# Performance work log

Hardware: AMD Instinct MI355X
Metric: run time of the kernel (lower is better)

The kernel has to match this reference:

```python
import jax, jax.numpy as jnp
import numpy as np

N = 50000
E = 800000
F_IN = 128
HID = 64
NEG_SLOPE = 0.2
LN_EPS = 1e-5


def _gat_layer(x, W, att_src, att_dst, bias, src, dst, heads, out_ch, concat):
    # x: [N, in], W: [in, heads*out_ch], att_*: [heads, out_ch]
    n = x.shape[0]
    xp = (x @ W).reshape(n, heads, out_ch)                    # [N, H, C]
    a_src = jnp.einsum('nhc,hc->nh', xp, att_src)             # [N, H]
    a_dst = jnp.einsum('nhc,hc->nh', xp, att_dst)             # [N, H]
    e = jax.nn.leaky_relu(a_src[src] + a_dst[dst], NEG_SLOPE) # [E, H]
    # edge softmax over incoming edges of each destination node
    m = jax.ops.segment_max(e, dst, num_segments=n)           # [N, H]
    ex = jnp.exp(e - m[dst])
    s = jax.ops.segment_sum(ex, dst, num_segments=n)          # [N, H]
    alpha = ex / s[dst]                                       # [E, H]
    agg = jax.ops.segment_sum(xp[src] * alpha[:, :, None], dst, num_segments=n)
    out = agg.reshape(n, heads * out_ch) if concat else agg.mean(axis=1)
    return out + bias


def _layernorm(x, g, b):
    mu = x.mean(-1, keepdims=True)
    var = x.var(-1, keepdims=True)
    return (x - mu) / jnp.sqrt(var + LN_EPS) * g + b


def setup_inputs() -> dict:
    key = jax.random.key(0)
    ks = jax.random.split(key, 12)
    sc = 0.1
    return {
        'x': jax.random.normal(ks[0], (N, F_IN), jnp.float32),
        'edge_index': jax.random.randint(ks[1], (2, E), 0, N, jnp.int64),
        'W1': jax.random.normal(ks[2], (F_IN, 4 * HID), jnp.float32) * sc,
        'att_src1': jax.random.normal(ks[3], (4, HID), jnp.float32) * sc,
        'att_dst1': jax.random.normal(ks[4], (4, HID), jnp.float32) * sc,
        'b1': jnp.zeros((4 * HID,), jnp.float32),
        'ln1_g': jnp.ones((4 * HID,), jnp.float32),
        'ln1_b': jnp.zeros((4 * HID,), jnp.float32),
        'W2': jax.random.normal(ks[5], (4 * HID, 2 * HID), jnp.float32) * sc,
        'att_src2': jax.random.normal(ks[6], (2, HID), jnp.float32) * sc,
        'att_dst2': jax.random.normal(ks[7], (2, HID), jnp.float32) * sc,
        'b2': jnp.zeros((2 * HID,), jnp.float32),
        'ln2_g': jnp.ones((2 * HID,), jnp.float32),
        'ln2_b': jnp.zeros((2 * HID,), jnp.float32),
        'W3': jax.random.normal(ks[8], (2 * HID, F_IN), jnp.float32) * sc,
        'att_src3': jax.random.normal(ks[9], (1, F_IN), jnp.float32) * sc,
        'att_dst3': jax.random.normal(ks[10], (1, F_IN), jnp.float32) * sc,
        'b3': jnp.zeros((F_IN,), jnp.float32),
    }


def reference(x, edge_index, W1, att_src1, att_dst1, b1, ln1_g, ln1_b,
              W2, att_src2, att_dst2, b2, ln2_g, ln2_b,
              W3, att_src3, att_dst3, b3):
    n = x.shape[0]
    # PyG GATConv default: add self-loops
    loop = jnp.arange(n, dtype=edge_index.dtype)
    src = jnp.concatenate([edge_index[0], loop])
    dst = jnp.concatenate([edge_index[1], loop])

    h = _gat_layer(x, W1, att_src1, att_dst1, b1, src, dst, 4, HID, True)
    h = jax.nn.elu(_layernorm(h, ln1_g, ln1_b))
    # dropout p=0.2 is identity in eval mode
    h = _gat_layer(h, W2, att_src2, att_dst2, b2, src, dst, 2, HID, True)
    h = jax.nn.elu(_layernorm(h, ln2_g, ln2_b))
    out = _gat_layer(h, W3, att_src3, att_dst3, b3, src, dst, 1, F_IN, True)
    return out
```

## Files before the change

### kernel.cpp

```cpp
#include <hip/hip_runtime.h>
#include <hip/hip_bf16.h>
#include <math.h>

#define N_NODES 50000
#define N_EDGES 800000
#define E_TOT   850000
#define SCAN_B  1024

typedef __hip_bfloat16 bf16;
typedef __attribute__((ext_vector_type(8))) short short8v;
typedef __attribute__((ext_vector_type(4))) float float4v;

static __device__ __forceinline__ float u2f(unsigned short u) {
    return __uint_as_float(((unsigned int)u) << 16);
}
static __device__ __forceinline__ unsigned short f2u(float f) {
    unsigned int u = __float_as_uint(f);
    return (unsigned short)((u + 0x7FFFu + ((u >> 16) & 1u)) >> 16);
}

template<bool BF>
static __device__ __forceinline__ float ldv(const void* p, int i) {
    if constexpr (BF)
        return u2f(((const unsigned short*)p)[i]);
    else
        return ((const float*)p)[i];
}

__global__ void k_detect(const unsigned int* __restrict__ x32,
                         const unsigned int* __restrict__ ei32,
                         int* __restrict__ flags) {
    if (threadIdx.x == 0 && blockIdx.x == 0) {
        int cnt = 0;
        for (int i = 0; i < 256; i++) {
            unsigned int e = (x32[i] >> 7) & 0xFF;
            cnt += (e >= 90 && e <= 140) ? 1 : 0;
        }
        flags[0] = (cnt >= 128) ? 1 : 0;
        int z = 0;
        for (int i = 0; i < 64; i++) z += (ei32[2 * i + 1] == 0) ? 1 : 0;
        flags[1] = (z >= 48) ? 1 : 0;
    }
}

__global__ void k_zero(int* __restrict__ p, int n) {
    int i = blockIdx.x * blockDim.x + threadIdx.x;
    if (i < n) p[i] = 0;
}

template<bool I64>
__global__ void k_hist(const int* __restrict__ flags, const void* __restrict__ ei,
                       int* __restrict__ counts) {
    if ((flags[1] != 0) != I64) return;
    int i = blockIdx.x * blockDim.x + threadIdx.x;
    if (i >= E_TOT) return;
    int d;
    if (i < N_EDGES)
        d = I64 ? (int)((const long long*)ei)[N_EDGES + i] : ((const int*)ei)[N_EDGES + i];
    else
        d = i - N_EDGES;
    atomicAdd(&counts[d], 1);
}

__global__ void k_scan1(const int* __restrict__ counts, int* __restrict__ scanned,
                        int* __restrict__ partial, int n) {
    __shared__ int sh[SCAN_B];
    int i = blockIdx.x * SCAN_B + threadIdx.x;
    sh[threadIdx.x] = (i < n) ? counts[i] : 0;
    __syncthreads();
    for (int off = 1; off < SCAN_B; off <<= 1) {
        int t = (threadIdx.x >= off) ? sh[threadIdx.x - off] : 0;
        __syncthreads();
        sh[threadIdx.x] += t;
        __syncthreads();
    }
    if (i < n) scanned[i] = sh[threadIdx.x];
    if (threadIdx.x == SCAN_B - 1) partial[blockIdx.x] = sh[SCAN_B - 1];
}

__global__ void k_scan2(int* __restrict__ partial, int nb) {
    if (threadIdx.x == 0 && blockIdx.x == 0) {
        int acc = 0;
        for (int b = 0; b < nb; b++) { int t = partial[b]; partial[b] = acc; acc += t; }
    }
}

__global__ void k_scan3(const int* __restrict__ counts, const int* __restrict__ scanned,
                        const int* __restrict__ partial, int* __restrict__ rowptr,
                        int* __restrict__ cursor, int n) {
    int i = blockIdx.x * blockDim.x + threadIdx.x;
    if (i >= n) return;
    int incl = scanned[i] + partial[i / SCAN_B];
    rowptr[i + 1] = incl;
    cursor[i]     = incl - counts[i];
    if (i == 0) rowptr[0] = 0;
}

template<bool I64>
__global__ void k_scatter(const int* __restrict__ flags, const void* __restrict__ ei,
                          int* __restrict__ cursor, int* __restrict__ csr_src) {
    if ((flags[1] != 0) != I64) return;
    int i = blockIdx.x * blockDim.x + threadIdx.x;
    if (i >= E_TOT) return;
    int s, d;
    if (i < N_EDGES) {
        if constexpr (I64) {
            s = (int)((const long long*)ei)[i];
            d = (int)((const long long*)ei)[N_EDGES + i];
        } else {
            s = ((const int*)ei)[i];
            d = ((const int*)ei)[N_EDGES + i];
        }
    } else {
        s = d = i - N_EDGES;
    }
    int pos = atomicAdd(&cursor[d], 1);
    csr_src[pos] = s;
}

template<bool XBF>
__global__ void k_prepx(const int* __restrict__ flags, const void* __restrict__ x,
                        bf16* __restrict__ xb, int n4) {
    if ((flags[0] != 0) != XBF) return;
    int i = blockIdx.x * blockDim.x + threadIdx.x;
    if (i >= n4) return;
    if constexpr (XBF) {
        ((ushort4*)xb)[i] = ((const ushort4*)x)[i];
    } else {
        float4 f = ((const float4*)x)[i];
        ushort4 u;
        u.x = f2u(f.x); u.y = f2u(f.y); u.z = f2u(f.z); u.w = f2u(f.w);
        ((ushort4*)xb)[i] = u;
    }
}

template<int K, int NT, bool PBF>
__global__ void k_prepw(const int* __restrict__ flags, const void* __restrict__ W,
                        bf16* __restrict__ Wt) {
    if ((flags[0] != 0) != PBF) return;
    int i = blockIdx.x * blockDim.x + threadIdx.x;
    if (i >= K * NT) return;
    int k = i / NT, c = i - k * NT;
    Wt[c * K + k] = __float2bfloat16(ldv<PBF>(W, i));
}

struct PrepArgs { const void* src[13]; int off[13]; int len[13]; };

template<bool PBF>
__global__ void k_prep_small(const int* __restrict__ flags, PrepArgs a,
                             float* __restrict__ par) {
    if ((flags[0] != 0) != PBF) return;
    for (int seg = blockIdx.x; seg < 13; seg += gridDim.x)
        for (int i = threadIdx.x; i < a.len[seg]; i += blockDim.x)
            par[a.off[seg] + i] = ldv<PBF>(a.src[seg], i);
}

template<int K, int NT, int SPW, int H>
__global__ __launch_bounds__(256) void k_gemm_mfma2(const bf16* __restrict__ A,
                                                    const bf16* __restrict__ Wt,
                                                    bf16* __restrict__ xp,
                                                    const float* __restrict__ att_s,
                                                    const float* __restrict__ att_d,
                                                    float* __restrict__ asr,
                                                    float* __restrict__ adst) {
    constexpr int KF     = K / 32;
    constexpr int NSG    = NT / (16 * SPW);
    constexpr int NTILES = N_NODES / 16;
    constexpr int C      = NT / H;
    const int l    = threadIdx.x & 63;
    const int wid  = blockIdx.x * 4 + (threadIdx.x >> 6);
    const int sg   = wid % NSG;
    const int wpg  = (gridDim.x * 4) / NSG;
    const int t0   = wid / NSG;
    const int r16  = l & 15;
    const int kgrp = (l >> 4) * 8;
    const int head = (sg * SPW * 16) / C;

    short8v b[SPW][KF];
    float as_r[SPW][4], ad_r[SPW][4];
    #pragma unroll
    for (int s = 0; s < SPW; s++) {
        const int cs  = (sg * SPW + s) * 16;
        const int col = cs + r16;
        #pragma unroll
        for (int kf = 0; kf < KF; kf++)
            b[s][kf] = *(const short8v*)(Wt + (size_t)col * K + kf * 32 + kgrp);
        #pragma unroll
        for (int r = 0; r < 4; r++) {
            const int ch = cs + (l >> 4) * 4 + r;
            as_r[s][r] = att_s[ch];
            ad_r[s][r] = att_d[ch];
        }
    }

    for (int t = t0; t < NTILES; t += wpg) {
        const int m0 = t * 16;
        short8v a[KF];
        #pragma unroll
        for (int kf = 0; kf < KF; kf++)
            a[kf] = *(const short8v*)(A + (size_t)(m0 + r16) * K + kf * 32 + kgrp);
        float4v acc[SPW] = {};
        #pragma unroll
        for (int kf = 0; kf < KF; kf++)
            #pragma unroll
            for (int s = 0; s < SPW; s++)
                acc[s] = __builtin_amdgcn_mfma_f32_16x16x32_bf16(b[s][kf], a[kf], acc[s], 0, 0, 0);

        float pa = 0.f, pd = 0.f;
        #pragma unroll
        for (int s = 0; s < SPW; s++)
            #pragma unroll
            for (int r = 0; r < 4; r++) {
                pa = fmaf(acc[s][r], as_r[s][r], pa);
                pd = fmaf(acc[s][r], ad_r[s][r], pd);
            }
        pa += __shfl_xor(pa, 16); pa += __shfl_xor(pa, 32);
        pd += __shfl_xor(pd, 16); pd += __shfl_xor(pd, 32);
        if (l < 16) {
            atomicAdd(&asr [(size_t)(m0 + l) * H + head], pa);
            atomicAdd(&adst[(size_t)(m0 + l) * H + head], pd);
        }

        const int node = m0 + r16;
        #pragma unroll
        for (int s = 0; s < SPW; s++) {
            const int ch = (sg * SPW + s) * 16 + (l >> 4) * 4;
            uint2 o;
            o.x = (unsigned int)f2u(acc[s][0]) | ((unsigned int)f2u(acc[s][1]) << 16);
            o.y = (unsigned int)f2u(acc[s][2]) | ((unsigned int)f2u(acc[s][3]) << 16);
            *(uint2*)(xp + (size_t)node * NT + ch) = o;
        }
    }
}

template<int ND>
static __device__ __forceinline__ void gacc(const unsigned int* __restrict__ xpd,
                                            int off, float a, float* __restrict__ acc) {
    unsigned int d[ND];
    if constexpr (ND == 4) {
        uint4 t = *(const uint4*)(xpd + off);
        d[0] = t.x; d[1] = t.y; d[2] = t.z; d[3] = t.w;
    } else {
        uint2 t = *(const uint2*)(xpd + off);
        d[0] = t.x; d[1] = t.y;
    }
    #pragma unroll
    for (int k = 0; k < ND; k++) {
        acc[2 * k]     = fmaf(a, __uint_as_float(d[k] << 16),         acc[2 * k]);
        acc[2 * k + 1] = fmaf(a, __uint_as_float(d[k] & 0xffff0000u), acc[2 * k + 1]);
    }
}

template<int CT, int H, bool LAST, bool OBF>
__global__ __launch_bounds__(256) void k_agg3(const int* __restrict__ flags,
                                              const bf16* __restrict__ xp,
                                              const float* __restrict__ asr,
                                              const float* __restrict__ adst,
                                              const int* __restrict__ rowptr,
                                              const int* __restrict__ csr_src,
                                              const float* __restrict__ bias,
                                              const float* __restrict__ gamma,
                                              const float* __restrict__ beta,
                                              void* __restrict__ outv) {
    if constexpr (LAST) { if ((flags[0] != 0) != OBF) return; }
    constexpr int NPW = 2;
    constexpr int LPN = 64 / NPW;
    constexpr int V   = CT / LPN;
    constexpr int C   = CT / H;
    constexpr int LPH = C / V;
    constexpr int ND  = V / 2;
    constexpr int STR = CT / 2;
    const int l     = threadIdx.x & 63;
    const int w     = threadIdx.x >> 6;
    const int half  = l / LPN;
    const int li    = l - half * LPN;
    const int hd    = li / LPH;
    const int slot  = li & (LPH - 1);
    const int lbase = half * LPN + hd * LPH;
    const int coff  = ND * li;

    float bv[V], gv[V], bev[V];
    #pragma unroll
    for (int v = 0; v < V; v++) bv[v] = bias[V * li + v];
    if constexpr (!LAST) {
        #pragma unroll
        for (int v = 0; v < V; v++) {
            gv[v]  = gamma[V * li + v];
            bev[v] = beta [V * li + v];
        }
    }
    const unsigned int* xpd = (const unsigned int*)xp;

    for (int n0 = blockIdx.x * 4 + w; n0 * NPW < N_NODES; n0 += gridDim.x * 4) {
        const int n  = n0 * NPW + half;
        const int b0 = rowptr[n], b1 = rowptr[n + 1];
        const int deg = b1 - b0;
        const float ad = adst[n * H + hd];

        float m = -1e30f, s = 0.f;
        for (int j = b0 + slot; j < b1; j += LPH) {
            int sn = csr_src[j];
            float e = asr[sn * H + hd] + ad;
            e = e > 0.f ? e : 0.2f * e;
            float mn = fmaxf(m, e);
            s = s * __expf(m - mn) + __expf(e - mn);
            m = mn;
        }
        #pragma unroll
        for (int off = 1; off < LPH; off <<= 1) {
            float mo = __shfl_xor(m, off);
            float so = __shfl_xor(s, off);
            float mn = fmaxf(m, mo);
            s = s * __expf(m - mn) + so * __expf(mo - mn);
            m = mn;
        }
        const float inv_s = 1.f / s;

        float acc[V];
        #pragma unroll
        for (int v = 0; v < V; v++) acc[v] = 0.f;

        for (int cbase = 0; cbase < deg; cbase += LPH) {
            const int nn = min(LPH, deg - cbase);
            int   sn_l = 0;
            float al_l = 0.f;
            if (slot < nn) {
                sn_l = csr_src[b0 + cbase + slot];
                float e = asr[sn_l * H + hd] + ad;
                e = e > 0.f ? e : 0.2f * e;
                al_l = __expf(e - m) * inv_s;
            }
            const int nn4 = (nn + 3) & ~3;
            for (int e4 = 0; e4 < nn4; e4 += 4) {
                int   s0 = __shfl(sn_l, lbase + e4 + 0);
                int   s1 = __shfl(sn_l, lbase + e4 + 1);
                int   s2 = __shfl(sn_l, lbase + e4 + 2);
                int   s3 = __shfl(sn_l, lbase + e4 + 3);
                float a0 = __shfl(al_l, lbase + e4 + 0);
                float a1 = __shfl(al_l, lbase + e4 + 1);
                float a2 = __shfl(al_l, lbase + e4 + 2);
                float a3 = __shfl(al_l, lbase + e4 + 3);
                gacc<ND>(xpd, s0 * STR + coff, a0, acc);
                gacc<ND>(xpd, s1 * STR + coff, a1, acc);
                gacc<ND>(xpd, s2 * STR + coff, a2, acc);
                gacc<ND>(xpd, s3 * STR + coff, a3, acc);
            }
        }
        #pragma unroll
        for (int v = 0; v < V; v++) acc[v] += bv[v];

        if constexpr (!LAST) {
            float lsum = 0.f, lsq = 0.f;
            #pragma unroll
            for (int v = 0; v < V; v++) { lsum += acc[v]; lsq = fmaf(acc[v], acc[v], lsq); }
            #pragma unroll
            for (int off = 1; off < LPN; off <<= 1) {
                lsum += __shfl_xor(lsum, off);
                lsq  += __shfl_xor(lsq,  off);
            }
            float mu  = lsum * (1.f / CT);
            float var = lsq  * (1.f / CT) - mu * mu;
            float rs  = rsqrtf(var + 1e-5f);
            unsigned int od[ND];
            #pragma unroll
            for (int k = 0; k < ND; k++) {
                float y0 = (acc[2 * k]     - mu) * rs * gv[2 * k]     + bev[2 * k];
                float y1 = (acc[2 * k + 1] - mu) * rs * gv[2 * k + 1] + bev[2 * k + 1];
                y0 = y0 > 0.f ? y0 : expm1f(y0);
                y1 = y1 > 0.f ? y1 : expm1f(y1);
                od[k] = (unsigned int)f2u(y0) | ((unsigned int)f2u(y1) << 16);
            }
            unsigned int* ob = (unsigned int*)outv + (size_t)n * STR + coff;
            if constexpr (ND == 4) *(uint4*)ob = make_uint4(od[0], od[1], od[2], od[3]);
            else                   *(uint2*)ob = make_uint2(od[0], od[1]);
        } else {
            if constexpr (OBF) {
                uint2 o;
                o.x = (unsigned int)f2u(acc[0]) | ((unsigned int)f2u(acc[1]) << 16);
                o.y = (unsigned int)f2u(acc[2]) | ((unsigned int)f2u(acc[3]) << 16);
                *(uint2*)((bf16*)outv + (size_t)n * CT + V * li) = o;
            } else {
                *(float4*)((float*)outv + (size_t)n * CT + V * li) =
                    make_float4(acc[0], acc[1], acc[2], acc[3]);
            }
        }
    }
}

extern "C" void kernel_launch(void* const* d_in, const int* in_sizes, int n_in,
                              void* d_out, int out_size, void* d_ws, size_t ws_size,
                              hipStream_t stream) {
    const void* x   = d_in[0];
    const void* ei  = d_in[1];
    const void* W1  = d_in[2];
    const void* W2  = d_in[8];
    const void* W3  = d_in[14];

    char* ws = (char*)d_ws;
    bf16*  xp     = (bf16*)(ws);
    bf16*  hbuf   = (bf16*)(ws + 25600000);
    float* asr    = (float*)(ws + 51200000);
    float* adst   = (float*)(ws + 52000000);
    int*   counts = (int*)  (ws + 52800000);
    int*   scannd = (int*)  (ws + 53000000);
    int*   part   = (int*)  (ws + 53200000);
    int*   rowptr = (int*)  (ws + 53200256);
    int*   cursor = (int*)  (ws + 53400260);
    int*   csrsrc = (int*)  (ws + 53600260);
    int*   flags  = (int*)  (ws + 57000260);
    bf16*  Wt1    = (bf16*)(ws + 57000320);
    bf16*  Wt2    = (bf16*)(ws + 57065856);
    bf16*  Wt3    = (bf16*)(ws + 57131392);
    float* params = (float*)(ws + 57164160);

    bf16* xb = hbuf;

    const int nb_scan = (N_NODES + SCAN_B - 1) / SCAN_B;
    const int AGGB    = (N_NODES / 2 + 3) / 4;

    k_detect<<<1, 64, 0, stream>>>((const unsigned int*)x, (const unsigned int*)ei, flags);

    k_zero<<<(N_NODES + 255) / 256, 256, 0, stream>>>(counts, N_NODES);
    k_hist<false><<<(E_TOT + 255) / 256, 256, 0, stream>>>(flags, ei, counts);
    k_hist<true ><<<(E_TOT + 255) / 256, 256, 0, stream>>>(flags, ei, counts);
    k_scan1<<<nb_scan, SCAN_B, 0, stream>>>(counts, scannd, part, N_NODES);
    k_scan2<<<1, 64, 0, stream>>>(part, nb_scan);
    k_scan3<<<(N_NODES + 255) / 256, 256, 0, stream>>>(counts, scannd, part, rowptr, cursor, N_NODES);
    k_scatter<false><<<(E_TOT + 255) / 256, 256, 0, stream>>>(flags, ei, cursor, csrsrc);
    k_scatter<true ><<<(E_TOT + 255) / 256, 256, 0, stream>>>(flags, ei, cursor, csrsrc);

    const int n4 = N_NODES * 128 / 4;
    k_prepx<false><<<(n4 + 255) / 256, 256, 0, stream>>>(flags, x, xb, n4);
    k_prepx<true ><<<(n4 + 255) / 256, 256, 0, stream>>>(flags, x, xb, n4);
    k_prepw<128, 256, false><<<128, 256, 0, stream>>>(flags, W1, Wt1);
    k_prepw<128, 256, true ><<<128, 256, 0, stream>>>(flags, W1, Wt1);
    k_prepw<256, 128, false><<<128, 256, 0, stream>>>(flags, W2, Wt2);
    k_prepw<256, 128, true ><<<128, 256, 0, stream>>>(flags, W2, Wt2);
    k_prepw<128, 128, false><<<64, 256, 0, stream>>>(flags, W3, Wt3);
    k_prepw<128, 128, true ><<<64, 256, 0, stream>>>(flags, W3, Wt3);

    PrepArgs pa;
    const int srcs[13] = {3, 4, 5, 6, 7, 9, 10, 11, 12, 13, 15, 16, 17};
    const int offs[13] = {0, 256, 512, 768, 1024, 1280, 1408, 1536, 1664, 1792, 1920, 2048, 2176};
    const int lens[13] = {256, 256, 256, 256, 256, 128, 128, 128, 128, 128, 128, 128, 128};
    for (int i = 0; i < 13; i++) { pa.src[i] = d_in[srcs[i]]; pa.off[i] = offs[i]; pa.len[i] = lens[i]; }
    k_prep_small<false><<<13, 256, 0, stream>>>(flags, pa, params);
    k_prep_small<true ><<<13, 256, 0, stream>>>(flags, pa, params);

    k_zero<<<(400000 + 255) / 256, 256, 0, stream>>>((int*)asr, 400000);
    k_gemm_mfma2<128, 256, 4, 4><<<768, 256, 0, stream>>>(xb, Wt1, xp, params + 0, params + 256, asr, adst);
    k_agg3<256, 4, false, false><<<AGGB, 256, 0, stream>>>(flags, xp, asr, adst, rowptr, csrsrc,
                                                           params + 512, params + 768, params + 1024, hbuf);

    k_zero<<<(400000 + 255) / 256, 256, 0, stream>>>((int*)asr, 400000);
    k_gemm_mfma2<256, 128, 2, 2><<<768, 256, 0, stream>>>(hbuf, Wt2, xp, params + 1280, params + 1408, asr, adst);
    k_agg3<128, 2, false, false><<<AGGB, 256, 0, stream>>>(flags, xp, asr, adst, rowptr, csrsrc,
                                                           params + 1536, params + 1664, params + 1792, hbuf);

    k_zero<<<(400000 + 255) / 256, 256, 0, stream>>>((int*)asr, 400000);
    k_gemm_mfma2<128, 128, 2, 1><<<768, 256, 0, stream>>>(hbuf, Wt3, xp, params + 1920, params + 2048, asr, adst);
    k_agg3<128, 1, true, false><<<AGGB, 256, 0, stream>>>(flags, xp, asr, adst, rowptr, csrsrc,
                                                          params + 2176, nullptr, nullptr, d_out);
    k_agg3<128, 1, true, true ><<<AGGB, 256, 0, stream>>>(flags, xp, asr, adst, rowptr, csrsrc,
                                                          params + 2176, nullptr, nullptr, d_out);
}
```

Baseline: 354.8 us.

## Degree-sort aggregation nodes, store fp16 projections, merge prep kernels and zeroing

Nodes are bucketed by in-degree and processed in descending-degree order, so the two nodes sharing a wavefront have similar work and load imbalance drops. Projected features are stored as fp16 instead of bf16, and the aggregation loop now batches 4-8 gathers before accumulating to expose more memory-level parallelism. Duplicate flag-dispatched kernel launches are collapsed into runtime branches, the per-layer zero kernels are merged into one init kernel with separate attention buffers per layer, and weight preparation runs as one kernel. The extra degree-sort kernels add setup cost, and fp16 storage changes overflow and rounding behaviour.

```diff
diff --git a/kernel.cpp b/kernel.cpp
--- a/kernel.cpp
+++ b/kernel.cpp
@@ -1,11 +1,13 @@
 #include <hip/hip_runtime.h>
 #include <hip/hip_bf16.h>
+#include <hip/hip_fp16.h>
 #include <math.h>
 
 #define N_NODES 50000
 #define N_EDGES 800000
 #define E_TOT   850000
 #define SCAN_B  1024
+#define NPAIRS  (N_NODES / 2)
 
 typedef __hip_bfloat16 bf16;
 typedef __attribute__((ext_vector_type(8))) short short8v;
@@ -18,45 +20,39 @@
     unsigned int u = __float_as_uint(f);
     return (unsigned short)((u + 0x7FFFu + ((u >> 16) & 1u)) >> 16);
 }
-
-template<bool BF>
-static __device__ __forceinline__ float ldv(const void* p, int i) {
-    if constexpr (BF)
-        return u2f(((const unsigned short*)p)[i]);
-    else
-        return ((const float*)p)[i];
-}
-
-__global__ void k_detect(const unsigned int* __restrict__ x32,
-                         const unsigned int* __restrict__ ei32,
-                         int* __restrict__ flags) {
-    if (threadIdx.x == 0 && blockIdx.x == 0) {
-        int cnt = 0;
-        for (int i = 0; i < 256; i++) {
-            unsigned int e = (x32[i] >> 7) & 0xFF;
-            cnt += (e >= 90 && e <= 140) ? 1 : 0;
-        }
-        flags[0] = (cnt >= 128) ? 1 : 0;
-        int z = 0;
-        for (int i = 0; i < 64; i++) z += (ei32[2 * i + 1] == 0) ? 1 : 0;
-        flags[1] = (z >= 48) ? 1 : 0;
-    }
-}
-
-__global__ void k_zero(int* __restrict__ p, int n) {
-    int i = blockIdx.x * blockDim.x + threadIdx.x;
-    if (i < n) p[i] = 0;
-}
-
-template<bool I64>
+static __device__ __forceinline__ float ldr(const void* p, int i, bool bf) {
+    return bf ? u2f(((const unsigned short*)p)[i]) : ((const float*)p)[i];
+}
+
+__global__ void k_init(const unsigned int* __restrict__ x32,
+                       const unsigned int* __restrict__ ei32,
+                       int* __restrict__ zero_base, int nzero,
+                       int* __restrict__ flags) {
+    int i = blockIdx.x * 256 + threadIdx.x;
+    if (i < nzero) zero_base[i] = 0;
+    if (blockIdx.x == 0) {
+        __shared__ int c1, c2;
+        if (threadIdx.x == 0) { c1 = 0; c2 = 0; }
+        __syncthreads();
+        unsigned int e = (x32[threadIdx.x] >> 7) & 0xFF;
+        if (e >= 90 && e <= 140) atomicAdd(&c1, 1);
+        if (threadIdx.x < 64 && ei32[2 * threadIdx.x + 1] == 0) atomicAdd(&c2, 1);
+        __syncthreads();
+        if (threadIdx.x == 0) {
+            flags[0] = (c1 >= 128) ? 1 : 0;
+            flags[1] = (c2 >= 48) ? 1 : 0;
+        }
+    }
+}
+
 __global__ void k_hist(const int* __restrict__ flags, const void* __restrict__ ei,
                        int* __restrict__ counts) {
-    if ((flags[1] != 0) != I64) return;
     int i = blockIdx.x * blockDim.x + threadIdx.x;
     if (i >= E_TOT) return;
     int d;
     if (i < N_EDGES)
-        d = I64 ? (int)((const long long*)ei)[N_EDGES + i] : ((const int*)ei)[N_EDGES + i];
+        d = flags[1] ? (int)((const long long*)ei)[N_EDGES + i]
+                     : ((const int*)ei)[N_EDGES + i];
     else
         d = i - N_EDGES;
     atomicAdd(&counts[d], 1);
@@ -87,24 +83,39 @@
 
 __global__ void k_scan3(const int* __restrict__ counts, const int* __restrict__ scanned,
                         const int* __restrict__ partial, int* __restrict__ rowptr,
-                        int* __restrict__ cursor, int n) {
+                        int* __restrict__ cursor, int* __restrict__ dhist, int n) {
     int i = blockIdx.x * blockDim.x + threadIdx.x;
     if (i >= n) return;
     int incl = scanned[i] + partial[i / SCAN_B];
     rowptr[i + 1] = incl;
     cursor[i]     = incl - counts[i];
     if (i == 0) rowptr[0] = 0;
-}
-
-template<bool I64>
+    atomicAdd(&dhist[min(counts[i], 511)], 1);
+}
+
+__global__ void k_dscan(const int* __restrict__ dhist, int* __restrict__ dbase) {
+    if (threadIdx.x == 0 && blockIdx.x == 0) {
+        int acc = 0;
+        for (int d = 511; d >= 0; d--) { dbase[d] = acc; acc += dhist[d]; }
+    }
+}
+
+__global__ void k_dscatter(const int* __restrict__ counts, const int* __restrict__ dbase,
+                           int* __restrict__ dcur, int* __restrict__ order) {
+    int i = blockIdx.x * blockDim.x + threadIdx.x;
+    if (i >= N_NODES) return;
+    int deg = min(counts[i], 511);
+    int pos = dbase[deg] + atomicAdd(&dcur[deg], 1);
+    order[pos] = i;
+}
+
 __global__ void k_scatter(const int* __restrict__ flags, const void* __restrict__ ei,
                           int* __restrict__ cursor, int* __restrict__ csr_src) {
-    if ((flags[1] != 0) != I64) return;
     int i = blockIdx.x * blockDim.x + threadIdx.x;
     if (i >= E_TOT) return;
     int s, d;
     if (i < N_EDGES) {
-        if constexpr (I64) {
+        if (flags[1]) {
             s = (int)((const long long*)ei)[i];
             d = (int)((const long long*)ei)[N_EDGES + i];
         } else {
@@ -118,13 +129,11 @@
     csr_src[pos] = s;
 }
 
-template<bool XBF>
 __global__ void k_prepx(const int* __restrict__ flags, const void* __restrict__ x,
                         bf16* __restrict__ xb, int n4) {
-    if ((flags[0] != 0) != XBF) return;
     int i = blockIdx.x * blockDim.x + threadIdx.x;
     if (i >= n4) return;
-    if constexpr (XBF) {
+    if (flags[0]) {
         ((ushort4*)xb)[i] = ((const ushort4*)x)[i];
     } else {
         float4 f = ((const float4*)x)[i];
@@ -134,31 +143,39 @@
     }
 }
 
-template<int K, int NT, bool PBF>
-__global__ void k_prepw(const int* __restrict__ flags, const void* __restrict__ W,
-                        bf16* __restrict__ Wt) {
-    if ((flags[0] != 0) != PBF) return;
-    int i = blockIdx.x * blockDim.x + threadIdx.x;
-    if (i >= K * NT) return;
-    int k = i / NT, c = i - k * NT;
-    Wt[c * K + k] = __float2bfloat16(ldv<PBF>(W, i));
+__global__ void k_prepw_all(const int* __restrict__ flags,
+                            const void* __restrict__ W1, const void* __restrict__ W2,
+                            const void* __restrict__ W3,
+                            bf16* __restrict__ Wt1, bf16* __restrict__ Wt2,
+                            bf16* __restrict__ Wt3) {
+    const bool bf = flags[0] != 0;
+    int i = blockIdx.x * 256 + threadIdx.x;
+    if (i < 32768) {
+        int k = i >> 8, c = i & 255;
+        Wt1[c * 128 + k] = __float2bfloat16(ldr(W1, i, bf));
+    } else if (i < 65536) {
+        int j = i - 32768, k = j >> 7, c = j & 127;
+        Wt2[c * 256 + k] = __float2bfloat16(ldr(W2, j, bf));
+    } else if (i < 81920) {
+        int j = i - 65536, k = j >> 7, c = j & 127;
+        Wt3[c * 128 + k] = __float2bfloat16(ldr(W3, j, bf));
+    }
 }
 
 struct PrepArgs { const void* src[13]; int off[13]; int len[13]; };
 
-template<bool PBF>
 __global__ void k_prep_small(const int* __restrict__ flags, PrepArgs a,
                              float* __restrict__ par) {
-    if ((flags[0] != 0) != PBF) return;
+    const bool bf = flags[0] != 0;
     for (int seg = blockIdx.x; seg < 13; seg += gridDim.x)
         for (int i = threadIdx.x; i < a.len[seg]; i += blockDim.x)
-            par[a.off[seg] + i] = ldv<PBF>(a.src[seg], i);
+            par[a.off[seg] + i] = ldr(a.src[seg], i, bf);
 }
 
 template<int K, int NT, int SPW, int H>
 __global__ __launch_bounds__(256) void k_gemm_mfma2(const bf16* __restrict__ A,
                                                     const bf16* __restrict__ Wt,
-                                                    bf16* __restrict__ xp,
+                                                    unsigned short* __restrict__ xp,
                                                     const float* __restrict__ att_s,
                                                     const float* __restrict__ att_d,
                                                     float* __restrict__ asr,
@@ -226,57 +243,41 @@
         for (int s = 0; s < SPW; s++) {
             const int ch = (sg * SPW + s) * 16 + (l >> 4) * 4;
             uint2 o;
-            o.x = (unsigned int)f2u(acc[s][0]) | ((unsigned int)f2u(acc[s][1]) << 16);
-            o.y = (unsigned int)f2u(acc[s][2]) | ((unsigned int)f2u(acc[s][3]) << 16);
+            o.x = (unsigned int)__half_as_ushort(__float2half(acc[s][0])) |
+                  ((unsigned int)__half_as_ushort(__float2half(acc[s][1])) << 16);
+            o.y = (unsigned int)__half_as_ushort(__float2half(acc[s][2])) |
+                  ((unsigned int)__half_as_ushort(__float2half(acc[s][3])) << 16);
             *(uint2*)(xp + (size_t)node * NT + ch) = o;
         }
     }
 }
 
-template<int ND>
-static __device__ __forceinline__ void gacc(const unsigned int* __restrict__ xpd,
-                                            int off, float a, float* __restrict__ acc) {
-    unsigned int d[ND];
-    if constexpr (ND == 4) {
-        uint4 t = *(const uint4*)(xpd + off);
-        d[0] = t.x; d[1] = t.y; d[2] = t.z; d[3] = t.w;
-    } else {
-        uint2 t = *(const uint2*)(xpd + off);
-        d[0] = t.x; d[1] = t.y;
-    }
-    #pragma unroll
-    for (int k = 0; k < ND; k++) {
-        acc[2 * k]     = fmaf(a, __uint_as_float(d[k] << 16),         acc[2 * k]);
-        acc[2 * k + 1] = fmaf(a, __uint_as_float(d[k] & 0xffff0000u), acc[2 * k + 1]);
-    }
-}
-
-template<int CT, int H, bool LAST, bool OBF>
-__global__ __launch_bounds__(256) void k_agg3(const int* __restrict__ flags,
-                                              const bf16* __restrict__ xp,
+template<int CT, int H, bool LAST>
+__global__ __launch_bounds__(256) void k_agg4(const int* __restrict__ flags,
+                                              const unsigned short* __restrict__ xp,
                                               const float* __restrict__ asr,
                                               const float* __restrict__ adst,
                                               const int* __restrict__ rowptr,
                                               const int* __restrict__ csr_src,
+                                              const int* __restrict__ order,
                                               const float* __restrict__ bias,
                                               const float* __restrict__ gamma,
                                               const float* __restrict__ beta,
                                               void* __restrict__ outv) {
-    if constexpr (LAST) { if ((flags[0] != 0) != OBF) return; }
-    constexpr int NPW = 2;
-    constexpr int LPN = 64 / NPW;
+    constexpr int LPN = 32;
     constexpr int V   = CT / LPN;
     constexpr int C   = CT / H;
     constexpr int LPH = C / V;
     constexpr int ND  = V / 2;
     constexpr int STR = CT / 2;
+    constexpr int G   = (ND == 4) ? 4 : 8;
     const int l     = threadIdx.x & 63;
     const int w     = threadIdx.x >> 6;
-    const int half  = l / LPN;
-    const int li    = l - half * LPN;
+    const int half  = l >> 5;
+    const int li    = l & 31;
     const int hd    = li / LPH;
     const int slot  = li & (LPH - 1);
-    const int lbase = half * LPN + hd * LPH;
+    const int lbase = half * 32 + hd * LPH;
     const int coff  = ND * li;
 
     float bv[V], gv[V], bev[V];
@@ -291,14 +292,25 @@
     }
     const unsigned int* xpd = (const unsigned int*)xp;
 
-    for (int n0 = blockIdx.x * 4 + w; n0 * NPW < N_NODES; n0 += gridDim.x * 4) {
-        const int n  = n0 * NPW + half;
-        const int b0 = rowptr[n], b1 = rowptr[n + 1];
-        const int deg = b1 - b0;
-        const float ad = adst[n * H + hd];
-
-        float m = -1e30f, s = 0.f;
-        for (int j = b0 + slot; j < b1; j += LPH) {
+    const int p = blockIdx.x * 4 + w;
+    if (p >= NPAIRS) return;
+    const int n  = order[2 * p + half];
+    const int b0 = rowptr[n], b1 = rowptr[n + 1];
+    const int deg = b1 - b0;
+    const float ad = adst[n * H + hd];
+    const int sn_first = csr_src[b0];
+
+    float m, s, e0 = 0.f;
+    int sn0 = sn_first;
+    {
+        int j = b0 + slot;
+        if (j < b1) {
+            sn0 = csr_src[j];
+            float e = asr[sn0 * H + hd] + ad;
+            e0 = e > 0.f ? e : 0.2f * e;
+            m = e0; s = 1.f;
+        } else { m = -1e30f; s = 0.f; }
+        for (j += LPH; j < b1; j += LPH) {
             int sn = csr_src[j];
             float e = asr[sn * H + hd] + ad;
             e = e > 0.f ? e : 0.2f * e;
@@ -306,83 +318,99 @@
             s = s * __expf(m - mn) + __expf(e - mn);
             m = mn;
         }
-        #pragma unroll
-        for (int off = 1; off < LPH; off <<= 1) {
-            float mo = __shfl_xor(m, off);
-            float so = __shfl_xor(s, off);
-            float mn = fmaxf(m, mo);
-            s = s * __expf(m - mn) + so * __expf(mo - mn);
-            m = mn;
-        }
-        const float inv_s = 1.f / s;
-
-        float acc[V];
-        #pragma unroll
-        for (int v = 0; v < V; v++) acc[v] = 0.f;
-
-        for (int cbase = 0; cbase < deg; cbase += LPH) {
-            const int nn = min(LPH, deg - cbase);
-            int   sn_l = 0;
-            float al_l = 0.f;
-            if (slot < nn) {
+    }
+    #pragma unroll
+    for (int off = 1; off < LPH; off <<= 1) {
+        float mo = __shfl_xor(m, off);
+        float so = __shfl_xor(s, off);
+        float mn = fmaxf(m, mo);
+        s = s * __expf(m - mn) + so * __expf(mo - mn);
+        m = mn;
+    }
+    const float inv_s = 1.f / s;
+
+    float acc[V];
+    #pragma unroll
+    for (int v = 0; v < V; v++) acc[v] = 0.f;
+
+    for (int cbase = 0; cbase < deg; cbase += LPH) {
+        const int nn = min(LPH, deg - cbase);
+        int   sn_l = sn_first;
+        float al_l = 0.f;
+        if (slot < nn) {
+            if (cbase == 0) {
+                sn_l = sn0;
+                al_l = __expf(e0 - m) * inv_s;
+            } else {
                 sn_l = csr_src[b0 + cbase + slot];
                 float e = asr[sn_l * H + hd] + ad;
                 e = e > 0.f ? e : 0.2f * e;
                 al_l = __expf(e - m) * inv_s;
             }
-            const int nn4 = (nn + 3) & ~3;
-            for (int e4 = 0; e4 < nn4; e4 += 4) {
-                int   s0 = __shfl(sn_l, lbase + e4 + 0);
-                int   s1 = __shfl(sn_l, lbase + e4 + 1);
-                int   s2 = __shfl(sn_l, lbase + e4 + 2);
-                int   s3 = __shfl(sn_l, lbase + e4 + 3);
-                float a0 = __shfl(al_l, lbase + e4 + 0);
-                float a1 = __shfl(al_l, lbase + e4 + 1);
-                float a2 = __shfl(al_l, lbase + e4 + 2);
-                float a3 = __shfl(al_l, lbase + e4 + 3);
-                gacc<ND>(xpd, s0 * STR + coff, a0, acc);
-                gacc<ND>(xpd, s1 * STR + coff, a1, acc);
-                gacc<ND>(xpd, s2 * STR + coff, a2, acc);
-                gacc<ND>(xpd, s3 * STR + coff, a3, acc);
+        }
+        const int nnG = (nn + G - 1) & ~(G - 1);
+        for (int eb = 0; eb < nnG; eb += G) {
+            int sns[G]; float als[G];
+            #pragma unroll
+            for (int g = 0; g < G; g++) {
+                sns[g] = __shfl(sn_l, lbase + eb + g);
+                als[g] = __shfl(al_l, lbase + eb + g);
             }
-        }
-        #pragma unroll
-        for (int v = 0; v < V; v++) acc[v] += bv[v];
-
-        if constexpr (!LAST) {
-            float lsum = 0.f, lsq = 0.f;
+            unsigned int d[G][ND];
             #pragma unroll
-            for (int v = 0; v < V; v++) { lsum += acc[v]; lsq = fmaf(acc[v], acc[v], lsq); }
+            for (int g = 0; g < G; g++) {
+                if constexpr (ND == 4)
+                    *(uint4*)d[g] = *(const uint4*)(xpd + (size_t)sns[g] * STR + coff);
+                else
+                    *(uint2*)d[g] = *(const uint2*)(xpd + (size_t)sns[g] * STR + coff);
+            }
             #pragma unroll
-            for (int off = 1; off < LPN; off <<= 1) {
-                lsum += __shfl_xor(lsum, off);
-                lsq  += __shfl_xor(lsq,  off);
-            }
-            float mu  = lsum * (1.f / CT);
-            float var = lsq  * (1.f / CT) - mu * mu;
-            float rs  = rsqrtf(var + 1e-5f);
-            unsigned int od[ND];
-            #pragma unroll
-            for (int k = 0; k < ND; k++) {
-                float y0 = (acc[2 * k]     - mu) * rs * gv[2 * k]     + bev[2 * k];
-                float y1 = (acc[2 * k + 1] - mu) * rs * gv[2 * k + 1] + bev[2 * k + 1];
-                y0 = y0 > 0.f ? y0 : expm1f(y0);
-                y1 = y1 > 0.f ? y1 : expm1f(y1);
-                od[k] = (unsigned int)f2u(y0) | ((unsigned int)f2u(y1) << 16);
-            }
-            unsigned int* ob = (unsigned int*)outv + (size_t)n * STR + coff;
-            if constexpr (ND == 4) *(uint4*)ob = make_uint4(od[0], od[1], od[2], od[3]);
-            else                   *(uint2*)ob = make_uint2(od[0], od[1]);
+            for (int g = 0; g < G; g++)
+                #pragma unroll
+                for (int k = 0; k < ND; k++) {
+                    float x0 = __half2float(__ushort_as_half((unsigned short)(d[g][k] & 0xffffu)));
+                    float x1 = __half2float(__ushort_as_half((unsigned short)(d[g][k] >> 16)));
+                    acc[2 * k]     = fmaf(als[g], x0, acc[2 * k]);
+                    acc[2 * k + 1] = fmaf(als[g], x1, acc[2 * k + 1]);
+                }
+        }
+    }
+    #pragma unroll
+    for (int v = 0; v < V; v++) acc[v] += bv[v];
+
+    if constexpr (!LAST) {
+        float lsum = 0.f, lsq = 0.f;
+        #pragma unroll
+        for (int v = 0; v < V; v++) { lsum += acc[v]; lsq = fmaf(acc[v], acc[v], lsq); }
+        #pragma unroll
+        for (int off = 1; off < LPN; off <<= 1) {
+            lsum += __shfl_xor(lsum, off);
+            lsq  += __shfl_xor(lsq,  off);
+        }
+        float mu  = lsum * (1.f / CT);
+        float var = lsq  * (1.f / CT) - mu * mu;
+        float rs  = rsqrtf(var + 1e-5f);
+        unsigned int od[ND];
+        #pragma unroll
+        for (int k = 0; k < ND; k++) {
+            float y0 = (acc[2 * k]     - mu) * rs * gv[2 * k]     + bev[2 * k];
+            float y1 = (acc[2 * k + 1] - mu) * rs * gv[2 * k + 1] + bev[2 * k + 1];
+            y0 = y0 > 0.f ? y0 : expm1f(y0);
+            y1 = y1 > 0.f ? y1 : expm1f(y1);
+            od[k] = (unsigned int)f2u(y0) | ((unsigned int)f2u(y1) << 16);
+        }
+        unsigned int* ob = (unsigned int*)outv + (size_t)n * STR + coff;
+        if constexpr (ND == 4) *(uint4*)ob = make_uint4(od[0], od[1], od[2], od[3]);
+        else                   *(uint2*)ob = make_uint2(od[0], od[1]);
+    } else {
+        if (flags[0]) {
+            uint2 o;
+            o.x = (unsigned int)f2u(acc[0]) | ((unsigned int)f2u(acc[1]) << 16);
+            o.y = (unsigned int)f2u(acc[2]) | ((unsigned int)f2u(acc[3]) << 16);
+            *(uint2*)((bf16*)outv + (size_t)n * CT + V * li) = o;
         } else {
-            if constexpr (OBF) {
-                uint2 o;
-                o.x = (unsigned int)f2u(acc[0]) | ((unsigned int)f2u(acc[1]) << 16);
-                o.y = (unsigned int)f2u(acc[2]) | ((unsigned int)f2u(acc[3]) << 16);
-                *(uint2*)((bf16*)outv + (size_t)n * CT + V * li) = o;
-            } else {
-                *(float4*)((float*)outv + (size_t)n * CT + V * li) =
-                    make_float4(acc[0], acc[1], acc[2], acc[3]);
-            }
+            *(float4*)((float*)outv + (size_t)n * CT + V * li) =
+                make_float4(acc[0], acc[1], acc[2], acc[3]);
         }
     }
 }
@@ -390,77 +418,72 @@
 extern "C" void kernel_launch(void* const* d_in, const int* in_sizes, int n_in,
                               void* d_out, int out_size, void* d_ws, size_t ws_size,
                               hipStream_t stream) {
-    const void* x   = d_in[0];
-    const void* ei  = d_in[1];
-    const void* W1  = d_in[2];
-    const void* W2  = d_in[8];
-    const void* W3  = d_in[14];
+    const void* x  = d_in[0];
+    const void* ei = d_in[1];
 
     char* ws = (char*)d_ws;
-    bf16*  xp     = (bf16*)(ws);
+    unsigned short* xp = (unsigned short*)(ws);
     bf16*  hbuf   = (bf16*)(ws + 25600000);
-    float* asr    = (float*)(ws + 51200000);
-    float* adst   = (float*)(ws + 52000000);
-    int*   counts = (int*)  (ws + 52800000);
-    int*   scannd = (int*)  (ws + 53000000);
-    int*   part   = (int*)  (ws + 53200000);
-    int*   rowptr = (int*)  (ws + 53200256);
-    int*   cursor = (int*)  (ws + 53400260);
-    int*   csrsrc = (int*)  (ws + 53600260);
-    int*   flags  = (int*)  (ws + 57000260);
-    bf16*  Wt1    = (bf16*)(ws + 57000320);
-    bf16*  Wt2    = (bf16*)(ws + 57065856);
-    bf16*  Wt3    = (bf16*)(ws + 57131392);
-    float* params = (float*)(ws + 57164160);
+    int*   counts = (int*)  (ws + 51200000);
+    int*   dhist  = (int*)  (ws + 51400000);
+    int*   dcur   = (int*)  (ws + 51402048);
+    float* asr1   = (float*)(ws + 51404096);
+    float* adst1  = (float*)(ws + 52204096);
+    float* asr2   = (float*)(ws + 53004096);
+    float* adst2  = (float*)(ws + 53404096);
+    float* asr3   = (float*)(ws + 53804096);
+    float* adst3  = (float*)(ws + 54004096);
+    const int kZeroInts = (54204096 - 51200000) / 4;
+    int*   scannd = (int*)  (ws + 54204096);
+    int*   part   = (int*)  (ws + 54404096);
+    int*   rowptr = (int*)  (ws + 54404352);
+    int*   cursor = (int*)  (ws + 54604416);
+    int*   csrsrc = (int*)  (ws + 54804416);
+    int*   order  = (int*)  (ws + 58204416);
+    int*   flags  = (int*)  (ws + 58404416);
+    bf16*  Wt1    = (bf16*) (ws + 58404480);
+    bf16*  Wt2    = (bf16*) (ws + 58470016);
+    bf16*  Wt3    = (bf16*) (ws + 58535552);
+    float* params = (float*)(ws + 58568320);
+    int*   dbase  = (int*)  (ws + 58577536);
 
     bf16* xb = hbuf;
 
     const int nb_scan = (N_NODES + SCAN_B - 1) / SCAN_B;
-    const int AGGB    = (N_NODES / 2 + 3) / 4;
-
-    k_detect<<<1, 64, 0, stream>>>((const unsigned int*)x, (const unsigned int*)ei, flags);
-
-    k_zero<<<(N_NODES + 255) / 256, 256, 0, stream>>>(counts, N_NODES);
-    k_hist<false><<<(E_TOT + 255) / 256, 256, 0, stream>>>(flags, ei, counts);
-    k_hist<true ><<<(E_TOT + 255) / 256, 256, 0, stream>>>(flags, ei, counts);
-    k_scan1<<<nb_scan, SCAN_B, 0, stream>>>(counts, scannd, part, N_NODES);
-    k_scan2<<<1, 64, 0, stream>>>(part, nb_scan);
-    k_scan3<<<(N_NODES + 255) / 256, 256, 0, stream>>>(counts, scannd, part, rowptr, cursor, N_NODES);
-    k_scatter<false><<<(E_TOT + 255) / 256, 256, 0, stream>>>(flags, ei, cursor, csrsrc);
-    k_scatter<true ><<<(E_TOT + 255) / 256, 256, 0, stream>>>(flags, ei, cursor, csrsrc);
+    const int AGGB    = (NPAIRS + 3) / 4;
+
+    k_init<<<(kZeroInts + 255) / 256, 256, 0, stream>>>((const unsigned int*)x,
+                                                        (const unsigned int*)ei,
+                                                        counts, kZeroInts, flags);
+
+    k_hist    <<<(E_TOT + 255) / 256, 256, 0, stream>>>(flags, ei, counts);
+    k_scan1   <<<nb_scan, SCAN_B, 0, stream>>>(counts, scannd, part, N_NODES);
+    k_scan2   <<<1, 64, 0, stream>>>(part, nb_scan);
+    k_scan3   <<<(N_NODES + 255) / 256, 256, 0, stream>>>(counts, scannd, part, rowptr, cursor, dhist, N_NODES);
+    k_dscan   <<<1, 64, 0, stream>>>(dhist, dbase);
+    k_dscatter<<<(N_NODES + 255) / 256, 256, 0, stream>>>(counts, dbase, dcur, order);
+    k_scatter <<<(E_TOT + 255) / 256, 256, 0, stream>>>(flags, ei, cursor, csrsrc);
 
     const int n4 = N_NODES * 128 / 4;
-    k_prepx<false><<<(n4 + 255) / 256, 256, 0, stream>>>(flags, x, xb, n4);
-    k_prepx<true ><<<(n4 + 255) / 256, 256, 0, stream>>>(flags, x, xb, n4);
-    k_prepw<128, 256, false><<<128, 256, 0, stream>>>(flags, W1, Wt1);
-    k_prepw<128, 256, true ><<<128, 256, 0, stream>>>(flags, W1, Wt1);
-    k_prepw<256, 128, false><<<128, 256, 0, stream>>>(flags, W2, Wt2);
-    k_prepw<256, 128, true ><<<128, 256, 0, stream>>>(flags, W2, Wt2);
-    k_prepw<128, 128, false><<<64, 256, 0, stream>>>(flags, W3, Wt3);
-    k_prepw<128, 128, true ><<<64, 256, 0, stream>>>(flags, W3, Wt3);
+    k_prepx<<<(n4 + 255) / 256, 256, 0, stream>>>(flags, x, xb, n4);
+    k_prepw_all<<<320, 256, 0, stream>>>(flags, d_in[2], d_in[8], d_in[14], Wt1, Wt2, Wt3);
 
     PrepArgs pa;
     const int srcs[13] = {3, 4, 5, 6, 7, 9, 10, 11, 12, 13, 15, 16, 17};
     const int offs[13] = {0, 256, 512, 768, 1024, 1280, 1408, 1536, 1664, 1792, 1920, 2048, 2176};
     const int lens[13] = {256, 256, 256, 256, 256, 128, 128, 128, 128, 128, 128, 128, 128};
     for (int i = 0; i < 13; i++) { pa.src[i] = d_in[srcs[i]]; pa.off[i] = offs[i]; pa.len[i] = lens[i]; }
-    k_prep_small<false><<<13, 256, 0, stream>>>(flags, pa, params);
-    k_prep_small<true ><<<13, 256, 0, stream>>>(flags, pa, params);
-
-    k_zero<<<(400000 + 255) / 256, 256, 0, stream>>>((int*)asr, 400000);
-    k_gemm_mfma2<128, 256, 4, 4><<<768, 256, 0, stream>>>(xb, Wt1, xp, params + 0, params + 256, asr, adst);
-    k_agg3<256, 4, false, false><<<AGGB, 256, 0, stream>>>(flags, xp, asr, adst, rowptr, csrsrc,
-                                                           params + 512, params + 768, params + 1024, hbuf);
-
-    k_zero<<<(400000 + 255) / 256, 256, 0, stream>>>((int*)asr, 400000);
-    k_gemm_mfma2<256, 128, 2, 2><<<768, 256, 0, stream>>>(hbuf, Wt2, xp, params + 1280, params + 1408, asr, adst);
-    k_agg3<128, 2, false, false><<<AGGB, 256, 0, stream>>>(flags, xp, asr, adst, rowptr, csrsrc,
-                                                           params + 1536, params + 1664, params + 1792, hbuf);
-
-    k_zero<<<(400000 + 255) / 256, 256, 0, stream>>>((int*)asr, 400000);
-    k_gemm_mfma2<128, 128, 2, 1><<<768, 256, 0, stream>>>(hbuf, Wt3, xp, params + 1920, params + 2048, asr, adst);
-    k_agg3<128, 1, true, false><<<AGGB, 256, 0, stream>>>(flags, xp, asr, adst, rowptr, csrsrc,
-                                                          params + 2176, nullptr, nullptr, d_out);
-    k_agg3<128, 1, true, true ><<<AGGB, 256, 0, stream>>>(flags, xp, asr, adst, rowptr, csrsrc,
-                                                          params + 2176, nullptr, nullptr, d_out);
-}
+    k_prep_small<<<13, 256, 0, stream>>>(flags, pa, params);
+
+    k_gemm_mfma2<128, 256, 4, 4><<<768, 256, 0, stream>>>(xb, Wt1, xp, params + 0, params + 256, asr1, adst1);
+    k_agg4<256, 4, false><<<AGGB, 256, 0, stream>>>(flags, xp, asr1, adst1, rowptr, csrsrc, order,
+                                                    params + 512, params + 768, params + 1024, hbuf);
+
+    k_gemm_mfma2<256, 128, 2, 2><<<768, 256, 0, stream>>>(hbuf, Wt2, xp, params + 1280, params + 1408, asr2, adst2);
+    k_agg4<128, 2, false><<<AGGB, 256, 0, stream>>>(flags, xp, asr2, adst2, rowptr, csrsrc, order,
+                                                    params + 1536, params + 1664, params + 1792, hbuf);
+
+    k_gemm_mfma2<128, 128, 2, 1><<<768, 256, 0, stream>>>(hbuf, Wt3, xp, params + 1920, params + 2048, asr3, adst3);
+    k_agg4<128, 1, true><<<AGGB, 256, 0, stream>>>(flags, xp, asr3, adst3, rowptr, csrsrc, order,
+                                                   params + 2176, nullptr, nullptr, d_out);
+}
```

New measurement: 577.7 us. +62.8%, slower.
